# Optimization experiments

Hardware: AMD Instinct MI355X
Metric: run time of the kernel (lower is better)

## Reference

```python
import jax, jax.numpy as jnp
import numpy as np

N = 10000; E = 320000
DIM = 176; ATT = 16; SH_HEADS = 16; TH = 4; NH = SH_HEADS + TH; VD = DIM // SH_HEADS
LMAX = 3; NSPH = (LMAX + 1) ** 2; ZDIM = 16; RDIM = 16
RSTART = 0.8; CUT = 5.0; NLAYERS = 2


def _ln(x):
    mu = jnp.mean(x, axis=-1, keepdims=True)
    dx = x - mu
    var = jnp.mean(dx ** 2, axis=-1, keepdims=True)
    return dx * (1e-6 + var) ** (-0.5)


def _sph(v):
    # real spherical harmonics up to l=3, unnormalized overall scale, [E,16]
    x, y, z = v[..., 0], v[..., 1], v[..., 2]
    s3 = np.float32(np.sqrt(3.0)); s15 = np.float32(np.sqrt(15.0))
    c1 = np.float32(np.sqrt(5.0 / 8.0)); c2 = np.float32(np.sqrt(3.0 / 8.0))
    x2, y2, z2 = x * x, y * y, z * z
    return jnp.stack([
        jnp.ones_like(x),
        x, y, z,
        s3 * x * y, s3 * y * z, 0.5 * (3.0 * z2 - 1.0), s3 * x * z, 0.5 * s3 * (x2 - y2),
        c1 * y * (3.0 * x2 - y2), s15 * x * y * z, c2 * y * (5.0 * z2 - 1.0),
        0.5 * z * (5.0 * z2 - 3.0), c2 * x * (5.0 * z2 - 1.0),
        0.5 * s15 * z * (x2 - y2), c1 * x * (x2 - 3.0 * y2),
    ], axis=-1)


def setup_inputs() -> dict:
    key = jax.random.key(0)
    ks = jax.random.split(key, 32)

    def rn(k, shape):
        fan_in = shape[0] if len(shape) > 1 else shape[0]
        return jax.random.normal(k, shape, dtype=jnp.float32) / np.float32(np.sqrt(shape[0]))

    species = jax.random.randint(ks[0], (N,), 0, 64)
    edge_src = jax.random.randint(ks[1], (E,), 0, N)
    edge_dst = jax.random.randint(ks[2], (E,), 0, N)
    distances = RSTART + (CUT - RSTART) * jax.random.uniform(ks[3], (E,), dtype=jnp.float32)
    raw = jax.random.normal(ks[4], (E, 3), dtype=jnp.float32)
    dirn = raw / jnp.linalg.norm(raw, axis=-1, keepdims=True)
    vec = dirn * distances[:, None]
    switch = 0.5 * (jnp.cos(jnp.pi * distances / CUT) + 1.0)

    inp = {
        'species': species, 'distances': distances, 'switch': switch,
        'edge_src': edge_src, 'edge_dst': edge_dst, 'vec': vec,
        'z_table': jax.random.normal(ks[5], (64, ZDIM), dtype=jnp.float32),
        'w_species': rn(ks[6], (ZDIM, DIM)),
        'pos_w1_0': rn(ks[7], (RDIM, 2 * ATT)), 'pos_b1_0': jnp.zeros((2 * ATT,), jnp.float32),
        'pos_w2_0': rn(ks[8], (2 * ATT, ATT)), 'pos_b2_0': jnp.zeros((ATT,), jnp.float32),
        'wq_0': rn(ks[9], (DIM, NH * ATT)), 'wk_0': rn(ks[10], (DIM, NH * ATT)),
        'wv_0': rn(ks[11], (DIM, SH_HEADS * VD)),
        'upd_w_0': rn(ks[12], (2 * DIM, DIM)), 'upd_b_0': jnp.zeros((DIM,), jnp.float32),
        'pos_w1_1': rn(ks[13], (RDIM + TH * (LMAX + 1), 2 * ATT)), 'pos_b1_1': jnp.zeros((2 * ATT,), jnp.float32),
        'pos_w2_1': rn(ks[14], (2 * ATT, ATT)), 'pos_b2_1': jnp.zeros((ATT,), jnp.float32),
        'wq_1': rn(ks[15], (DIM, NH * ATT)), 'wk_1': rn(ks[16], (DIM, NH * ATT)),
        'wv_1': rn(ks[17], (DIM, SH_HEADS * VD)),
        'upd_w_1': rn(ks[18], (2 * DIM, DIM)), 'upd_b_1': jnp.zeros((DIM,), jnp.float32),
    }
    return inp


def reference(species, distances, switch, edge_src, edge_dst, vec,
              z_table, w_species,
              pos_w1_0, pos_b1_0, pos_w2_0, pos_b2_0, wq_0, wk_0, wv_0, upd_w_0, upd_b_0,
              pos_w1_1, pos_b1_1, pos_w2_1, pos_b2_1, wq_1, wk_1, wv_1, upd_w_1, upd_b_1):
    Nn = species.shape[0]
    Zi = z_table[species]                      # [N, ZDIM] species encoding
    xi = _ln(Zi @ w_species)                   # [N, DIM]

    vhat = vec / distances[:, None]
    Yij = _sph(vhat)                           # [E, NSPH]
    ls = np.repeat(np.arange(LMAX + 1), 2 * np.arange(LMAX + 1) + 1)
    parity = jnp.asarray(((-1.0) ** ls).astype(np.float32))  # [NSPH]

    centers = jnp.linspace(RSTART, CUT, RDIM, dtype=jnp.float32)
    sigma = np.float32((CUT - RSTART) / (RDIM - 1))
    radial = jnp.exp(-(((distances[:, None] - centers) / sigma) ** 2))  # [E, RDIM]

    Vi = jnp.zeros((Nn, TH, NSPH), jnp.float32)
    pos = [(pos_w1_0, pos_b1_0, pos_w2_0, pos_b2_0), (pos_w1_1, pos_b1_1, pos_w2_1, pos_b2_1)]
    att = [(wq_0, wk_0, wv_0, upd_w_0, upd_b_0), (wq_1, wk_1, wv_1, upd_w_1, upd_b_1)]
    inv_sqrt_d = np.float32(1.0 / np.sqrt(ATT))

    for layer in range(NLAYERS):
        pw1, pb1, pw2, pb2 = pos[layer]
        wq, wk, wv, uw, ub = att[layer]
        if layer == 0:
            ur = radial
        else:
            # tensor relative positional features: [E, TH, NSPH]
            xij2 = (Vi[edge_dst] + (parity * Vi)[edge_src]) * Yij[:, None, :]
            us = [xij2[:, :, l * l:(l + 1) * (l + 1)].sum(axis=-1) for l in range(LMAX + 1)]
            ur = jnp.concatenate([radial] + us, axis=-1)
        w = jax.nn.swish(ur @ pw1 + pb1) @ pw2 + pb2     # [E, ATT] positional encoding
        q = (xi @ wq).reshape(Nn, NH, ATT)
        k = (xi @ wk).reshape(Nn, NH, ATT)
        # multiplicative relative positional attention coefficients [E, NH]
        aij = jnp.einsum('ehd,ed->eh', q[edge_dst] * k[edge_src], w) * (switch[:, None] * inv_sqrt_d)
        a_s, a_t = aij[:, :SH_HEADS], aij[:, SH_HEADS:]
        v = (xi @ wv).reshape(Nn, SH_HEADS, VD)
        mi = jax.ops.segment_sum(a_s[:, :, None] * v[edge_src], edge_dst, num_segments=Nn)  # [N,SH,VD]
        Vi = Vi + jax.ops.segment_sum(
            a_t[:, :, None] * (Yij[:, None, :] + parity * Vi[edge_src]), edge_dst, num_segments=Nn)
        ui = jnp.concatenate([xi, mi.reshape(Nn, -1)], axis=-1)
        xi = _ln(xi + ui @ uw + ub)
    return xi
```

## Files before the change

### kernel.cpp

```cpp
#include <hip/hip_runtime.h>
#include <hip/hip_bf16.h>
#include <math.h>

#define N_NODES 10000
#define N_PAD   10048
#define N_EDGES 320000
#define DIM     176
#define ATT     16
#define SH_HEADS 16
#define THH     4
#define NH      20
#define VD      11
#define ZDIM    16
#define RDIM    16
#define QK_W    (NH*ATT)
#define QKV_W   816
#define UI_W    (2*DIM)
#define KQ      192
#define SIGINV  3.5714285714285716f
#define RSTEP   0.28f

typedef unsigned short ushort_t;
typedef __attribute__((ext_vector_type(8))) short bf16x8;
typedef __attribute__((ext_vector_type(4))) float f32x4;


__device__ __forceinline__ ushort_t f2bf(float f) {
    __hip_bfloat16 b = __float2bfloat16(f);
    return *(ushort_t*)&b;
}

__device__ __forceinline__ float bf2f(ushort_t u) {
    return __uint_as_float(((unsigned)u) << 16);
}

__device__ __forceinline__ void sph16(float x, float y, float z, float* Y) {
    const float s3  = 1.7320508075688772f;
    const float s15 = 3.872983346207417f;
    const float c1  = 0.7905694150420949f;
    const float c2  = 0.6123724356957945f;
    float x2 = x*x, y2 = y*y, z2 = z*z;
    Y[0]  = 1.0f;
    Y[1]  = x;
    Y[2]  = y;
    Y[3]  = z;
    Y[4]  = s3 * x * y;
    Y[5]  = s3 * y * z;
    Y[6]  = 0.5f * (3.0f * z2 - 1.0f);
    Y[7]  = s3 * x * z;
    Y[8]  = 0.5f * s3 * (x2 - y2);
    Y[9]  = c1 * y * (3.0f * x2 - y2);
    Y[10] = s15 * x * y * z;
    Y[11] = c2 * y * (5.0f * z2 - 1.0f);
    Y[12] = 0.5f * z * (5.0f * z2 - 3.0f);
    Y[13] = c2 * x * (5.0f * z2 - 1.0f);
    Y[14] = 0.5f * s15 * z * (x2 - y2);
    Y[15] = c1 * x * (x2 - 3.0f * y2);
}

__device__ __forceinline__ void unpack8(const uint4 u, float* f) {
    f[0] = __uint_as_float(u.x << 16);
    f[1] = __uint_as_float(u.x & 0xffff0000u);
    f[2] = __uint_as_float(u.y << 16);
    f[3] = __uint_as_float(u.y & 0xffff0000u);
    f[4] = __uint_as_float(u.z << 16);
    f[5] = __uint_as_float(u.z & 0xffff0000u);
    f[6] = __uint_as_float(u.w << 16);
    f[7] = __uint_as_float(u.w & 0xffff0000u);
}


__global__ __launch_bounds__(256) void k_deg(const int* __restrict__ edst,
        const int* __restrict__ esrc, const float* __restrict__ dist,
        const float* __restrict__ swit, const float* __restrict__ vec,
        int* deg, int* rank, uint4* pk) {
    int e = blockIdx.x * 256 + threadIdx.x;
    if (e >= N_EDGES) return;
    int t_ = edst[e];
    rank[e] = atomicAdd(&deg[t_], 1);
    uint4 a, b;
    a.x = (unsigned)esrc[e];
    a.y = (unsigned)t_;
    a.z = __float_as_uint(dist[e]);
    a.w = __float_as_uint(swit[e]);
    b.x = __float_as_uint(vec[(size_t)e*3 + 0]);
    b.y = __float_as_uint(vec[(size_t)e*3 + 1]);
    b.z = __float_as_uint(vec[(size_t)e*3 + 2]);
    b.w = 0u;
    pk[(size_t)e*2 + 0] = a;
    pk[(size_t)e*2 + 1] = b;
}

__global__ __launch_bounds__(1024) void k_scan1(const int* deg, int* incl, int* bsum) {
    __shared__ int sd[1024];
    int b = blockIdx.x, tid = threadIdx.x;
    int gi = b * 1024 + tid;
    int v = (gi < N_NODES) ? deg[gi] : 0;
    sd[tid] = v;
    __syncthreads();
    for (int s = 1; s < 1024; s <<= 1) {
        int add = (tid >= s) ? sd[tid - s] : 0;
        __syncthreads();
        sd[tid] += add;
        __syncthreads();
    }
    if (gi < N_NODES) incl[gi] = sd[tid];
    if (tid == 1023) bsum[b] = sd[1023];
}

__global__ __launch_bounds__(1024) void k_scan3(const int* deg, const int* incl, const int* bsum,
                                                int* off) {
    __shared__ int bpre_s;
    int b = blockIdx.x, tid = threadIdx.x;
    if (tid == 0) {
        int acc = 0;
        for (int k = 0; k < b; k++) acc += bsum[k];
        bpre_s = acc;
    }
    __syncthreads();
    int gi = b * 1024 + tid;
    if (gi < N_NODES) {
        off[gi + 1] = bpre_s + incl[gi];
    }
    if (gi == 0) off[0] = 0;
}

__global__ __launch_bounds__(256) void k_perm(const int* edst, const int* rank,
                                              const int* off, int* perm) {
    int e = blockIdx.x * 256 + threadIdx.x;
    if (e >= N_EDGES) return;
    perm[off[edst[e]] + rank[e]] = e;
}

__global__ __launch_bounds__(256) void k_build(const int* __restrict__ perm,
        const uint4* __restrict__ pk,
        int* src_c, int* dst_c, float* dist_c, float* sc_c, float* Yf) {
    int p = blockIdx.x * 256 + threadIdx.x;
    if (p >= N_EDGES) return;
    int e  = perm[p];
    uint4 a = pk[(size_t)e*2 + 0];
    uint4 b = pk[(size_t)e*2 + 1];
    int s  = (int)a.x;
    int t_ = (int)a.y;
    float d  = __uint_as_float(a.z);
    float sw = __uint_as_float(a.w);
    float inv = 1.0f / d;
    float vx = __uint_as_float(b.x) * inv;
    float vy = __uint_as_float(b.y) * inv;
    float vz = __uint_as_float(b.z) * inv;
    src_c[p]  = s;
    dst_c[p]  = t_;
    dist_c[p] = d;
    sc_c[p]   = sw * 0.25f;
    float Y[16];
    sph16(vx, vy, vz, Y);
    #pragma unroll
    for (int m = 0; m < 16; m += 4)
        *(float4*)&Yf[(size_t)p * 16 + m] = make_float4(Y[m], Y[m+1], Y[m+2], Y[m+3]);
}


__device__ __forceinline__ void prep_qkv_body(int bid, int tid, const float* wq,
        const float* wk, const float* wv, ushort_t* Wtq) {
    int id = bid * 256 + tid;
    if (id >= 832 * KQ) return;
    int n = id / KQ, k = id - (id / KQ) * KQ;
    float v = 0.0f;
    if (k < DIM && n < QKV_W)
        v = (n < 320) ? wq[k * 320 + n] : (n < 640) ? wk[k * 320 + (n - 320)]
                                                    : wv[k * DIM + (n - 640)];
    Wtq[id] = f2bf(v);
}

__device__ __forceinline__ void prep_upd_body(int bid, int tid, const float* uw, ushort_t* Wtu) {
    int id = bid * 256 + tid;
    if (id >= 192 * UI_W) return;
    int n = id / UI_W, k = id - (id / UI_W) * UI_W;
    float v = (n < DIM) ? uw[k * DIM + n] : 0.0f;
    Wtu[id] = f2bf(v);
}

__device__ __forceinline__ void prep_mlp_body(int bid, int tid, const float* pw1,
        const float* pw2, ushort_t* w1T, ushort_t* w2T, int K1) {
    int id = bid * 256 + tid;
    if (id < 1024) {
        int n = id >> 5, k = id & 31;
        w1T[n * 32 + k] = (k < K1) ? f2bf(pw1[k * 32 + n]) : 0;
    } else if (id < 1536) {
        int id2 = id - 1024;
        int n = id2 >> 5, k = id2 & 31;
        w2T[n * 32 + k] = f2bf(pw2[k * 16 + n]);
    }
}

__global__ __launch_bounds__(256) void k_prep_all(
        const float* wq0, const float* wk0, const float* wv0, ushort_t* Wtq0,
        const float* wq1, const float* wk1, const float* wv1, ushort_t* Wtq1,
        const float* uw0, ushort_t* Wtu0, const float* uw1, ushort_t* Wtu1,
        const float* pw1_0, const float* pw2_0, ushort_t* w1T0, ushort_t* w2T0,
        const float* pw1_1, const float* pw2_1, ushort_t* w1T1, ushort_t* w2T1) {
    int bid = blockIdx.x, tid = threadIdx.x;
    if (bid < 624)        prep_qkv_body(bid,        tid, wq0, wk0, wv0, Wtq0);
    else if (bid < 1248)  prep_qkv_body(bid - 624,  tid, wq1, wk1, wv1, Wtq1);
    else if (bid < 1512)  prep_upd_body(bid - 1248, tid, uw0, Wtu0);
    else if (bid < 1776)  prep_upd_body(bid - 1512, tid, uw1, Wtu1);
    else if (bid < 1782)  prep_mlp_body(bid - 1776, tid, pw1_0, pw2_0, w1T0, w2T0, 16);
    else if (bid < 1788)  prep_mlp_body(bid - 1782, tid, pw1_1, pw2_1, w1T1, w2T1, 32);
}


template<int KCHUNKS>
__global__ __launch_bounds__(256) void k_gemm(const ushort_t* __restrict__ A, int sA,
                                              const ushort_t* __restrict__ Bt, int sB,
                                              float* __restrict__ Cv, int sC, int M, int N) {
    __shared__ ushort_t As[64 * 40];
    __shared__ ushort_t Bs[64 * 40];
    int tid  = threadIdx.x;
    int m0   = blockIdx.y * 64, n0 = blockIdx.x * 64;
    int w    = tid >> 6, lane = tid & 63, quad = lane >> 4, c16 = lane & 15;
    int arow = tid >> 2, aseg = tid & 3;
    f32x4 acc[4] = {};
    for (int kc = 0; kc < KCHUNKS; kc++) {
        int k0 = kc * 32;
        *(uint4*)&As[arow * 40 + aseg * 8] =
            *(const uint4*)&A[(size_t)(m0 + arow) * sA + k0 + aseg * 8];
        *(uint4*)&Bs[arow * 40 + aseg * 8] =
            *(const uint4*)&Bt[(size_t)(n0 + arow) * sB + k0 + aseg * 8];
        __syncthreads();
        bf16x8 a = *(const bf16x8*)&As[(w * 16 + c16) * 40 + quad * 8];
        #pragma unroll
        for (int t = 0; t < 4; t++) {
            bf16x8 b = *(const bf16x8*)&Bs[(t * 16 + c16) * 40 + quad * 8];
            acc[t] = __builtin_amdgcn_mfma_f32_16x16x32_bf16(a, b, acc[t], 0, 0, 0);
        }
        __syncthreads();
    }
    #pragma unroll
    for (int t = 0; t < 4; t++) {
        #pragma unroll
        for (int r = 0; r < 4; r++) {
            int row = m0 + w * 16 + quad * 4 + r;
            int col = n0 + t * 16 + c16;
            if (row < M && col < N)
                Cv[(size_t)row * sC + col] = acc[t][r];
        }
    }
}


__global__ __launch_bounds__(256) void k_gemmq(const ushort_t* __restrict__ A,
                                               const ushort_t* __restrict__ Bt,
                                               ushort_t* __restrict__ qh,
                                               ushort_t* __restrict__ kh,
                                               ushort_t* __restrict__ vh) {
    __shared__ ushort_t As[64 * 200];
    __shared__ ushort_t Bs[64 * 200];
    int tid  = threadIdx.x;
    int m0   = blockIdx.y * 64, n0 = blockIdx.x * 64;
    int w    = tid >> 6, lane = tid & 63, quad = lane >> 4, c16 = lane & 15;
    #pragma unroll
    for (int it = 0; it < 6; it++) {
        int seg = it * 256 + tid;
        int r = seg / 24, cs = seg - (seg / 24) * 24;
        *(uint4*)&As[r * 200 + cs * 8] =
            *(const uint4*)&A[(size_t)(m0 + r) * KQ + cs * 8];
        *(uint4*)&Bs[r * 200 + cs * 8] =
            *(const uint4*)&Bt[(size_t)(n0 + r) * KQ + cs * 8];
    }
    __syncthreads();
    f32x4 acc[4] = {};
    #pragma unroll
    for (int kc = 0; kc < 6; kc++) {
        bf16x8 a = *(const bf16x8*)&As[(w * 16 + c16) * 200 + kc * 32 + quad * 8];
        #pragma unroll
        for (int t = 0; t < 4; t++) {
            bf16x8 b = *(const bf16x8*)&Bs[(t * 16 + c16) * 200 + kc * 32 + quad * 8];
            acc[t] = __builtin_amdgcn_mfma_f32_16x16x32_bf16(a, b, acc[t], 0, 0, 0);
        }
    }
    #pragma unroll
    for (int t = 0; t < 4; t++) {
        #pragma unroll
        for (int r = 0; r < 4; r++) {
            int row = m0 + w * 16 + quad * 4 + r;
            int col = n0 + t * 16 + c16;
            if (row < N_NODES && col < QKV_W) {
                ushort_t bv = f2bf(acc[t][r]);
                if (col < 320)      qh[(size_t)row * QK_W + col] = bv;
                else if (col < 640) kh[(size_t)row * QK_W + (col - 320)] = bv;
                else                vh[(size_t)row * DIM  + (col - 640)] = bv;
            }
        }
    }
}


__global__ __launch_bounds__(256) void k_node_init(const int* species, const float* z_table,
                                                   const float* wsp, float* xi,
                                                   ushort_t* xib, ushort_t* cxm) {
    __shared__ float zs[16 * ZDIM];
    __shared__ float yt[16 * DIM];
    __shared__ float red[256];
    __shared__ float mus[16], rstds[16];
    int base = blockIdx.x * 16;
    int tid  = threadIdx.x;
    { int n = tid >> 4, kk = tid & 15;
      zs[tid] = z_table[species[base + n] * ZDIM + kk]; }
    __syncthreads();
    int c = tid;
    if (c < DIM) {
        float acc[16];
        #pragma unroll
        for (int n = 0; n < 16; n++) acc[n] = 0.0f;
        for (int kk = 0; kk < ZDIM; kk++) {
            float w = wsp[kk * DIM + c];
            #pragma unroll
            for (int n = 0; n < 16; n++) acc[n] += zs[n * ZDIM + kk] * w;
        }
        #pragma unroll
        for (int n = 0; n < 16; n++) yt[n * DIM + c] = acc[n];
    }
    __syncthreads();
    { int n2 = tid >> 4, j = tid & 15;
      float s = 0.0f;
      for (int c2 = j; c2 < DIM; c2 += 16) s += yt[n2 * DIM + c2];
      red[tid] = s; }
    __syncthreads();
    if (tid < 16) { float s = 0; for (int j = 0; j < 16; j++) s += red[tid * 16 + j]; mus[tid] = s / (float)DIM; }
    __syncthreads();
    { int n2 = tid >> 4, j = tid & 15;
      float mu = mus[n2], s = 0.0f;
      for (int c2 = j; c2 < DIM; c2 += 16) { float d = yt[n2 * DIM + c2] - mu; s += d * d; }
      red[tid] = s; }
    __syncthreads();
    if (tid < 16) { float s = 0; for (int j = 0; j < 16; j++) s += red[tid * 16 + j]; rstds[tid] = rsqrtf(s / (float)DIM + 1e-6f); }
    __syncthreads();
    if (c < DIM) {
        #pragma unroll
        for (int n = 0; n < 16; n++) {
            float val = (yt[n * DIM + c] - mus[n]) * rstds[n];
            xi[(size_t)(base + n) * DIM + c] = val;
            ushort_t bv = f2bf(val);
            xib[(size_t)(base + n) * KQ + c]   = bv;
            cxm[(size_t)(base + n) * UI_W + c] = bv;
        }
    } else if (c < KQ) {
        #pragma unroll
        for (int n = 0; n < 16; n++) xib[(size_t)(base + n) * KQ + c] = 0;
    }
}


template<bool L0>
__global__ __launch_bounds__(256) void k_edge(const float* dist_c, const float* sc_c,
        const int* src_c, const int* dst_c, const float* Yf, const ushort_t* Vih,
        const ushort_t* qh, const ushort_t* kh,
        const ushort_t* w1T, const float* pb1, const ushort_t* w2T, const float* pb2,
        ushort_t* aijh) {
    __shared__ ushort_t urS[64 * 40];
    __shared__ ushort_t Ht[4][16 * 40];
    __shared__ float    wdS[64 * 17];
    __shared__ ushort_t aS[NH][64];
    int tid  = threadIdx.x;
    int w    = tid >> 6, lane = tid & 63, quad = lane >> 4, c16 = lane & 15;
    int eb   = blockIdx.x * 64;

    int le = tid >> 2, part = tid & 3;
    int ie = eb + le;
    int sE = src_c[ie], tE = dst_c[ie];

    if (!L0) {
        int e  = tid & 63, tp = tid >> 6;
        int i  = eb + e;
        float d = dist_c[i];
        ushort_t ur4[4];
        #pragma unroll
        for (int r0 = 0; r0 < 4; r0++) {
            int r = tp * 4 + r0;
            float cc = 0.8f + (float)r * RSTEP;
            float uu = (d - cc) * SIGINV;
            ur4[r0] = f2bf(__expf(-uu * uu));
        }
        *(uint2*)&urS[e * 40 + tp * 4] = *(uint2*)ur4;
        float Y[16];
        #pragma unroll
        for (int m = 0; m < 16; m += 4) {
            float4 y = *(const float4*)&Yf[(size_t)i * 16 + m];
            Y[m] = y.x; Y[m+1] = y.y; Y[m+2] = y.z; Y[m+3] = y.w;
        }
        int s = src_c[i], t_ = dst_c[i];
        const uint4* vd4 = (const uint4*)(Vih + (size_t)t_ * 64);
        const uint4* vs4 = (const uint4*)(Vih + (size_t)s  * 64);
        int th = tp;
        float fd[16], fs[16];
        unpack8(vd4[2*th],   fd);     unpack8(vd4[2*th+1], fd+8);
        unpack8(vs4[2*th],   fs);     unpack8(vs4[2*th+1], fs+8);
        float us0 = (fd[0] + fs[0]) * Y[0];
        float us1 = 0.0f, us2 = 0.0f, us3 = 0.0f;
        #pragma unroll
        for (int m = 1; m < 4; m++)  us1 += (fd[m] - fs[m]) * Y[m];
        #pragma unroll
        for (int m = 4; m < 9; m++)  us2 += (fd[m] + fs[m]) * Y[m];
        #pragma unroll
        for (int m = 9; m < 16; m++) us3 += (fd[m] - fs[m]) * Y[m];
        urS[e * 40 + 16 + 0 * 4 + th] = f2bf(us0);
        urS[e * 40 + 16 + 1 * 4 + th] = f2bf(us1);
        urS[e * 40 + 16 + 2 * 4 + th] = f2bf(us2);
        urS[e * 40 + 16 + 3 * 4 + th] = f2bf(us3);
        __syncthreads();
    }

    uint4 kr[10];
    {
        const uint4* kseg = (const uint4*)(kh + (size_t)sE * QK_W) + part * 10;
        #pragma unroll
        for (int j = 0; j < 10; j++) kr[j] = kseg[j];
    }

    {
        int e0 = eb + w * 16;
        bf16x8 a1;
        if (L0) {
            float d = dist_c[e0 + c16];
            #pragma unroll
            for (int j = 0; j < 8; j++) {
                int r = quad * 8 + j;
                float v = 0.0f;
                if (r < 16) { float cc = 0.8f + (float)r * RSTEP; float uu = (d - cc) * SIGINV; v = __expf(-uu * uu); }
                a1[j] = (short)f2bf(v);
            }
        } else {
            a1 = *(const bf16x8*)&urS[(w * 16 + c16) * 40 + quad * 8];
        }
        bf16x8 b0 = *(const bf16x8*)&w1T[c16 * 32 + quad * 8];
        bf16x8 b1 = *(const bf16x8*)&w1T[(16 + c16) * 32 + quad * 8];
        f32x4 acc0 = {}, acc1 = {};
        acc0 = __builtin_amdgcn_mfma_f32_16x16x32_bf16(a1, b0, acc0, 0, 0, 0);
        acc1 = __builtin_amdgcn_mfma_f32_16x16x32_bf16(a1, b1, acc1, 0, 0, 0);
        float bb0 = pb1[c16], bb1 = pb1[c16 + 16];
        #pragma unroll
        for (int r = 0; r < 4; r++) {
            int er = quad * 4 + r;
            float h0 = acc0[r] + bb0; h0 = h0 / (1.0f + __expf(-h0));
            float h1 = acc1[r] + bb1; h1 = h1 / (1.0f + __expf(-h1));
            Ht[w][er * 40 + c16]      = f2bf(h0);
            Ht[w][er * 40 + 16 + c16] = f2bf(h1);
        }
        __syncthreads();
        bf16x8 a2 = *(const bf16x8*)&Ht[w][c16 * 40 + quad * 8];
        bf16x8 b2 = *(const bf16x8*)&w2T[c16 * 32 + quad * 8];
        f32x4 acc2 = {};
        acc2 = __builtin_amdgcn_mfma_f32_16x16x32_bf16(a2, b2, acc2, 0, 0, 0);
        float bb2 = pb2[c16];
        #pragma unroll
        for (int r = 0; r < 4; r++) {
            int er = quad * 4 + r;
            wdS[(w * 16 + er) * 17 + c16] = (acc2[r] + bb2) * sc_c[e0 + er];
        }
    }
    __syncthreads();

    {
        float wd[16];
        #pragma unroll
        for (int p = 0; p < 16; p++) wd[p] = wdS[le * 17 + p];
        const uint4* q4 = (const uint4*)(qh + (size_t)tE * QK_W) + part * 10;
        #pragma unroll
        for (int j = 0; j < 5; j++) {
            int h = part * 5 + j;
            float qa[8], qb[8], ka[8], kb[8];
            unpack8(q4[2*j],   qa); unpack8(q4[2*j+1], qb);
            unpack8(kr[2*j],   ka); unpack8(kr[2*j+1], kb);
            float acc = 0.0f;
            #pragma unroll
            for (int dd = 0; dd < 8; dd++) acc += qa[dd] * ka[dd] * wd[dd];
            #pragma unroll
            for (int dd = 0; dd < 8; dd++) acc += qb[dd] * kb[dd] * wd[8 + dd];
            aS[h][le] = f2bf(acc);
        }
    }
    __syncthreads();
    {
        const uint* aSw = (const uint*)aS;
        for (int idx = tid; idx < NH * 32; idx += 256) {
            int h = idx >> 5, w2 = idx & 31;
            *(uint*)(aijh + (size_t)h * N_EDGES + eb + w2 * 2) = aSw[h * 32 + w2];
        }
    }
}


__device__ __forceinline__ void mi_step(int i, int c0, bool f1, bool f2,
        const int* src_c, const ushort_t* aA, const ushort_t* aB, const ushort_t* vh,
        float& acc0, float& acc1, float& acc2, float& acc3) {
    int s0 = src_c[i];
    uint2 v0 = *(const uint2*)(vh + (size_t)s0 * DIM + c0);
    float a00 = bf2f(aA[i]), a0B = bf2f(aB[i]);
    float g01 = f1 ? a0B : a00, g02 = f2 ? a0B : a00;
    acc0 += a00 * __uint_as_float(v0.x << 16);
    acc1 += g01 * __uint_as_float(v0.x & 0xffff0000u);
    acc2 += g02 * __uint_as_float(v0.y << 16);
    acc3 += a0B * __uint_as_float(v0.y & 0xffff0000u);
}

__device__ __forceinline__ void mi_wave(int n, int lane, const int* off, const int* src_c,
        const ushort_t* aijh, const ushort_t* vh, ushort_t* cxm) {
    if (lane >= 44) return;
    int c0 = lane * 4;
    int hA = c0 / VD;
    int hB = (c0 + 3) / VD;
    bool f1 = ((c0 + 1) / VD) != hA;
    bool f2 = ((c0 + 2) / VD) != hA;
    const ushort_t* aA = aijh + (size_t)hA * N_EDGES;
    const ushort_t* aB = aijh + (size_t)hB * N_EDGES;
    int start = off[n], end = off[n + 1];
    float acc0 = 0, acc1 = 0, acc2 = 0, acc3 = 0;
    int cnt = end - start;
    int i = start;

#define MI_ACC(vv, av, bv) { \
    float aa = bf2f(av), ab = bf2f(bv); \
    float g1 = f1 ? ab : aa, g2 = f2 ? ab : aa; \
    acc0 += aa * __uint_as_float((vv).x << 16); \
    acc1 += g1 * __uint_as_float((vv).x & 0xffff0000u); \
    acc2 += g2 * __uint_as_float((vv).y << 16); \
    acc3 += ab * __uint_as_float((vv).y & 0xffff0000u); }

    if (cnt >= 4) {
        int iend = start + (cnt & ~3);
        int s0 = src_c[i], s1 = src_c[i+1], s2 = src_c[i+2], s3 = src_c[i+3];
        uint2 v0 = *(const uint2*)(vh + (size_t)s0 * DIM + c0);
        uint2 v1 = *(const uint2*)(vh + (size_t)s1 * DIM + c0);
        uint2 v2 = *(const uint2*)(vh + (size_t)s2 * DIM + c0);
        uint2 v3 = *(const uint2*)(vh + (size_t)s3 * DIM + c0);
        ushort_t pA0 = aA[i], pA1 = aA[i+1], pA2 = aA[i+2], pA3 = aA[i+3];
        ushort_t pB0 = aB[i], pB1 = aB[i+1], pB2 = aB[i+2], pB3 = aB[i+3];
        for (i += 4; i + 4 <= iend; i += 4) {
            int t0 = src_c[i], t1 = src_c[i+1], t2 = src_c[i+2], t3 = src_c[i+3];
            uint2 w0 = *(const uint2*)(vh + (size_t)t0 * DIM + c0);
            uint2 w1 = *(const uint2*)(vh + (size_t)t1 * DIM + c0);
            uint2 w2 = *(const uint2*)(vh + (size_t)t2 * DIM + c0);
            uint2 w3 = *(const uint2*)(vh + (size_t)t3 * DIM + c0);
            ushort_t qA0 = aA[i], qA1 = aA[i+1], qA2 = aA[i+2], qA3 = aA[i+3];
            ushort_t qB0 = aB[i], qB1 = aB[i+1], qB2 = aB[i+2], qB3 = aB[i+3];
            MI_ACC(v0, pA0, pB0); MI_ACC(v1, pA1, pB1);
            MI_ACC(v2, pA2, pB2); MI_ACC(v3, pA3, pB3);
            v0 = w0; v1 = w1; v2 = w2; v3 = w3;
            pA0 = qA0; pA1 = qA1; pA2 = qA2; pA3 = qA3;
            pB0 = qB0; pB1 = qB1; pB2 = qB2; pB3 = qB3;
        }
        MI_ACC(v0, pA0, pB0); MI_ACC(v1, pA1, pB1);
        MI_ACC(v2, pA2, pB2); MI_ACC(v3, pA3, pB3);
    }
    for (; i < end; i++)
        mi_step(i, c0, f1, f2, src_c, aA, aB, vh, acc0, acc1, acc2, acc3);
#undef MI_ACC
    ushort_t o[4] = {f2bf(acc0), f2bf(acc1), f2bf(acc2), f2bf(acc3)};
    *(uint2*)(cxm + (size_t)n * UI_W + DIM + c0) = *(uint2*)o;
}

__device__ __forceinline__ void vi_wave(int n, int lane, const int* off,
        const float* Yf, const ushort_t* aijh, ushort_t* Vih) {
    int th = lane >> 4, sm = lane & 15;
    const ushort_t* ah = aijh + (size_t)(SH_HEADS + th) * N_EDGES;
    int start = off[n], end = off[n + 1];
    float acc = 0.0f;
    int cnt = end - start;
    int i = start;
    if (cnt >= 4) {
        int iend = start + (cnt & ~3);
        float a0 = bf2f(ah[i]),   y0 = Yf[(size_t)i * 16 + sm];
        float a1 = bf2f(ah[i+1]), y1 = Yf[(size_t)(i+1) * 16 + sm];
        float a2 = bf2f(ah[i+2]), y2 = Yf[(size_t)(i+2) * 16 + sm];
        float a3 = bf2f(ah[i+3]), y3 = Yf[(size_t)(i+3) * 16 + sm];
        for (i += 4; i + 4 <= iend; i += 4) {
            float b0 = bf2f(ah[i]),   z0 = Yf[(size_t)i * 16 + sm];
            float b1 = bf2f(ah[i+1]), z1 = Yf[(size_t)(i+1) * 16 + sm];
            float b2 = bf2f(ah[i+2]), z2 = Yf[(size_t)(i+2) * 16 + sm];
            float b3 = bf2f(ah[i+3]), z3 = Yf[(size_t)(i+3) * 16 + sm];
            acc += a0 * y0 + a1 * y1 + a2 * y2 + a3 * y3;
            a0 = b0; a1 = b1; a2 = b2; a3 = b3;
            y0 = z0; y1 = z1; y2 = z2; y3 = z3;
        }
        acc += a0 * y0 + a1 * y1 + a2 * y2 + a3 * y3;
    }
    for (; i < end; i++)
        acc += bf2f(ah[i]) * Yf[(size_t)i * 16 + sm];
    Vih[(size_t)n * 64 + lane] = f2bf(acc);
}

__global__ __launch_bounds__(256) void k_agg0(const int* off, const int* src_c,
        const float* Yf, const ushort_t* aijh, const ushort_t* vh,
        ushort_t* cxm, ushort_t* Vih) {
    int wid  = blockIdx.x * 4 + (threadIdx.x >> 6);
    int lane = threadIdx.x & 63;
    if (wid < N_NODES)
        mi_wave(wid, lane, off, src_c, aijh, vh, cxm);
    else
        vi_wave(wid - N_NODES, lane, off, Yf, aijh, Vih);
}

__global__ __launch_bounds__(256) void k_agg1(const int* off, const int* src_c,
        const ushort_t* aijh, const ushort_t* vh, ushort_t* cxm) {
    int wid  = blockIdx.x * 4 + (threadIdx.x >> 6);
    int lane = threadIdx.x & 63;
    mi_wave(wid, lane, off, src_c, aijh, vh, cxm);
}


__global__ __launch_bounds__(256) void k_lnfinal(const float* yg, const float* xi,
        const float* ub, float* xo, ushort_t* xib, ushort_t* cxm) {
    __shared__ float yt[16 * DIM];
    __shared__ float red[256];
    __shared__ float mus[16], rstds[16];
    int base = blockIdx.x * 16;
    int tid  = threadIdx.x;
    for (int idx = tid; idx < 16 * DIM; idx += 256) {
        int n = idx / DIM, c = idx - n * DIM;
        yt[idx] = xi[(size_t)(base + n) * DIM + c]
                + yg[(size_t)(base + n) * DIM + c] + ub[c];
    }
    __syncthreads();
    { int n2 = tid >> 4, j = tid & 15;
      float s = 0.0f;
      for (int c2 = j; c2 < DIM; c2 += 16) s += yt[n2 * DIM + c2];
      red[tid] = s; }
    __syncthreads();
    if (tid < 16) { float s = 0; for (int j = 0; j < 16; j++) s += red[tid * 16 + j]; mus[tid] = s / (float)DIM; }
    __syncthreads();
    { int n2 = tid >> 4, j = tid & 15;
      float mu = mus[n2], s = 0.0f;
      for (int c2 = j; c2 < DIM; c2 += 16) { float d = yt[n2 * DIM + c2] - mu; s += d * d; }
      red[tid] = s; }
    __syncthreads();
    if (tid < 16) { float s = 0; for (int j = 0; j < 16; j++) s += red[tid * 16 + j]; rstds[tid] = rsqrtf(s / (float)DIM + 1e-6f); }
    __syncthreads();
    int c = tid;
    if (c < DIM) {
        #pragma unroll
        for (int n = 0; n < 16; n++) {
            float val = (yt[n * DIM + c] - mus[n]) * rstds[n];
            xo[(size_t)(base + n) * DIM + c] = val;
            ushort_t bv = f2bf(val);
            xib[(size_t)(base + n) * KQ + c]   = bv;
            cxm[(size_t)(base + n) * UI_W + c] = bv;
        }
    } else if (c < KQ) {
        #pragma unroll
        for (int n = 0; n < 16; n++) xib[(size_t)(base + n) * KQ + c] = 0;
    }
}


extern "C" void kernel_launch(void* const* d_in, const int* in_sizes, int n_in,
                              void* d_out, int out_size, void* d_ws, size_t ws_size,
                              hipStream_t stream) {
    const int*   species = (const int*)  d_in[0];
    const float* dist    = (const float*)d_in[1];
    const float* swit    = (const float*)d_in[2];
    const int*   esrc    = (const int*)  d_in[3];
    const int*   edst    = (const int*)  d_in[4];
    const float* vec     = (const float*)d_in[5];
    const float* z_table = (const float*)d_in[6];
    const float* wsp     = (const float*)d_in[7];
    const float* pw1_0 = (const float*)d_in[8],  *pb1_0 = (const float*)d_in[9];
    const float* pw2_0 = (const float*)d_in[10], *pb2_0 = (const float*)d_in[11];
    const float* wq0 = (const float*)d_in[12], *wk0 = (const float*)d_in[13];
    const float* wv0 = (const float*)d_in[14], *uw0 = (const float*)d_in[15];
    const float* ub0 = (const float*)d_in[16];
    const float* pw1_1 = (const float*)d_in[17], *pb1_1 = (const float*)d_in[18];
    const float* pw2_1 = (const float*)d_in[19], *pb2_1 = (const float*)d_in[20];
    const float* wq1 = (const float*)d_in[21], *wk1 = (const float*)d_in[22];
    const float* wv1 = (const float*)d_in[23], *uw1 = (const float*)d_in[24];
    const float* ub1 = (const float*)d_in[25];
    float* out = (float*)d_out;

    char* p = (char*)d_ws;
    auto alloc = [&](size_t bytes) -> char* {
        char* r = p;
        p += (bytes + 255) & ~(size_t)255;
        return r;
    };
    int* deg    = (int*)alloc((size_t)N_NODES * 4);
    int* incl   = (int*)alloc((size_t)N_NODES * 4);
    int* bsum   = (int*)alloc(64);
    int* off    = (int*)alloc((size_t)(N_NODES + 1) * 4);
    int* rank   = (int*)alloc((size_t)N_EDGES * 4);
    int* perm   = (int*)alloc((size_t)N_EDGES * 4);
    uint4* pk   = (uint4*)alloc((size_t)N_EDGES * 32);
    int*   src_c  = (int*)  alloc((size_t)N_EDGES * 4);
    int*   dst_c  = (int*)  alloc((size_t)N_EDGES * 4);
    float* dist_c = (float*)alloc((size_t)N_EDGES * 4);
    float* sc_c   = (float*)alloc((size_t)N_EDGES * 4);
    float* Yf     = (float*)alloc((size_t)N_EDGES * 16 * 4);
    float* xiA  = (float*)alloc((size_t)N_NODES * DIM * 4);
    float* xiB  = (float*)alloc((size_t)N_NODES * DIM * 4);
    ushort_t* xib  = (ushort_t*)alloc((size_t)N_PAD * KQ * 2);
    ushort_t* cxm  = (ushort_t*)alloc((size_t)N_PAD * UI_W * 2);
    ushort_t* qh   = (ushort_t*)alloc((size_t)N_NODES * QK_W * 2);
    ushort_t* kh   = (ushort_t*)alloc((size_t)N_NODES * QK_W * 2);
    ushort_t* vh   = (ushort_t*)alloc((size_t)N_NODES * DIM * 2);
    float* ybuf    = (float*)alloc((size_t)N_NODES * DIM * 4);
    ushort_t* Wtq0 = (ushort_t*)alloc((size_t)832 * KQ * 2);
    ushort_t* Wtq1 = (ushort_t*)alloc((size_t)832 * KQ * 2);
    ushort_t* Wtu0 = (ushort_t*)alloc((size_t)192 * UI_W * 2);
    ushort_t* Wtu1 = (ushort_t*)alloc((size_t)192 * UI_W * 2);
    ushort_t* w1T0 = (ushort_t*)alloc((size_t)32 * 32 * 2);
    ushort_t* w2T0 = (ushort_t*)alloc((size_t)16 * 32 * 2);
    ushort_t* w1T1 = (ushort_t*)alloc((size_t)32 * 32 * 2);
    ushort_t* w2T1 = (ushort_t*)alloc((size_t)16 * 32 * 2);
    ushort_t* Vih  = (ushort_t*)alloc((size_t)N_NODES * 64 * 2);
    ushort_t* aijh = (ushort_t*)alloc((size_t)N_EDGES * NH * 2);

    const int NB_E  = (N_EDGES + 255) / 256;
    const int NB_F  = N_EDGES / 64;
    const int NB_T  = N_NODES / 16;
    const dim3 GRID_QKV(13, 157);
    const dim3 GRID_UPD(3, 157);

    hipMemsetAsync(deg, 0, (size_t)N_NODES * 4, stream);
    k_deg<<<NB_E, 256, 0, stream>>>(edst, esrc, dist, swit, vec, deg, rank, pk);
    k_scan1<<<10, 1024, 0, stream>>>(deg, incl, bsum);
    k_scan3<<<10, 1024, 0, stream>>>(deg, incl, bsum, off);
    k_perm<<<NB_E, 256, 0, stream>>>(edst, rank, off, perm);
    k_build<<<NB_E, 256, 0, stream>>>(perm, pk, src_c, dst_c, dist_c, sc_c, Yf);

    k_prep_all<<<1788, 256, 0, stream>>>(wq0, wk0, wv0, Wtq0, wq1, wk1, wv1, Wtq1,
                                         uw0, Wtu0, uw1, Wtu1,
                                         pw1_0, pw2_0, w1T0, w2T0,
                                         pw1_1, pw2_1, w1T1, w2T1);

    k_node_init<<<NB_T, 256, 0, stream>>>(species, z_table, wsp, xiA, xib, cxm);

    k_gemmq<<<GRID_QKV, 256, 0, stream>>>(xib, Wtq0, qh, kh, vh);
    k_edge<true><<<NB_F, 256, 0, stream>>>(dist_c, sc_c, src_c, dst_c, Yf, Vih,
                                           qh, kh, w1T0, pb1_0, w2T0, pb2_0, aijh);
    k_agg0<<<5000, 256, 0, stream>>>(off, src_c, Yf, aijh, vh, cxm, Vih);
    k_gemm<11><<<GRID_UPD, 256, 0, stream>>>(cxm, UI_W, Wtu0, UI_W, ybuf, DIM,
                                             N_NODES, DIM);
    k_lnfinal<<<NB_T, 256, 0, stream>>>(ybuf, xiA, ub0, xiB, xib, cxm);

    k_gemmq<<<GRID_QKV, 256, 0, stream>>>(xib, Wtq1, qh, kh, vh);
    k_edge<false><<<NB_F, 256, 0, stream>>>(dist_c, sc_c, src_c, dst_c, Yf, Vih,
                                            qh, kh, w1T1, pb1_1, w2T1, pb2_1, aijh);
    k_agg1<<<2500, 256, 0, stream>>>(off, src_c, aijh, vh, cxm);
    k_gemm<11><<<GRID_UPD, 256, 0, stream>>>(cxm, UI_W, Wtu1, UI_W, ybuf, DIM,
                                             N_NODES, DIM);
    k_lnfinal<<<NB_T, 256, 0, stream>>>(ybuf, xiB, ub1, out, xib, cxm);
}
```

Before: 373.1 us.

## Fuse update GEMM with layernorm, merge preprocessing launches, single-block scan

The node-update GEMM and the residual layernorm become one kernel, k_updln. Each 64-row block stages its A rows in LDS, runs MFMA over all 176 output columns, and does the mean and variance reduction with lane shuffles. This removes the fp32 ybuf round trip and one launch per layer. Degree counting, weight prep and node init are merged into one multi-role kernel, and the two-kernel scan becomes a single 1024-thread block. The trade-offs: k_updln launches only 157 blocks and reads B straight from global memory, and every block of the merged pre-kernel reserves the init LDS.

```diff
diff --git a/kernel.cpp b/kernel.cpp
--- a/kernel.cpp
+++ b/kernel.cpp
@@ -70,11 +70,11 @@
 }
 
 
-__global__ __launch_bounds__(256) void k_deg(const int* __restrict__ edst,
-        const int* __restrict__ esrc, const float* __restrict__ dist,
-        const float* __restrict__ swit, const float* __restrict__ vec,
-        int* deg, int* rank, uint4* pk) {
-    int e = blockIdx.x * 256 + threadIdx.x;
+__device__ __forceinline__ void deg_body(int bid, int tid,
+        const int* __restrict__ edst, const int* __restrict__ esrc,
+        const float* __restrict__ dist, const float* __restrict__ swit,
+        const float* __restrict__ vec, int* deg, int* rank, uint4* pk) {
+    int e = bid * 256 + tid;
     if (e >= N_EDGES) return;
     int t_ = edst[e];
     rank[e] = atomicAdd(&deg[t_], 1);
@@ -91,38 +91,147 @@
     pk[(size_t)e*2 + 1] = b;
 }
 
-__global__ __launch_bounds__(1024) void k_scan1(const int* deg, int* incl, int* bsum) {
+__device__ __forceinline__ void prep_qkv_body(int bid, int tid, const float* wq,
+        const float* wk, const float* wv, ushort_t* Wtq) {
+    int id = bid * 256 + tid;
+    if (id >= 832 * KQ) return;
+    int n = id / KQ, k = id - (id / KQ) * KQ;
+    float v = 0.0f;
+    if (k < DIM && n < QKV_W)
+        v = (n < 320) ? wq[k * 320 + n] : (n < 640) ? wk[k * 320 + (n - 320)]
+                                                    : wv[k * DIM + (n - 640)];
+    Wtq[id] = f2bf(v);
+}
+
+__device__ __forceinline__ void prep_upd_body(int bid, int tid, const float* uw, ushort_t* Wtu) {
+    int id = bid * 256 + tid;
+    if (id >= 192 * UI_W) return;
+    int n = id / UI_W, k = id - (id / UI_W) * UI_W;
+    float v = (n < DIM) ? uw[k * DIM + n] : 0.0f;
+    Wtu[id] = f2bf(v);
+}
+
+__device__ __forceinline__ void prep_mlp_body(int bid, int tid, const float* pw1,
+        const float* pw2, ushort_t* w1T, ushort_t* w2T, int K1) {
+    int id = bid * 256 + tid;
+    if (id < 1024) {
+        int n = id >> 5, k = id & 31;
+        w1T[n * 32 + k] = (k < K1) ? f2bf(pw1[k * 32 + n]) : 0;
+    } else if (id < 1536) {
+        int id2 = id - 1024;
+        int n = id2 >> 5, k = id2 & 31;
+        w2T[n * 32 + k] = f2bf(pw2[k * 16 + n]);
+    }
+}
+
+struct InitSmem {
+    float zs[16 * ZDIM];
+    float yt[16 * DIM];
+    float red[256];
+    float mus[16], rstds[16];
+};
+
+__device__ void init_body(int bid, int tid, InitSmem& sm,
+        const int* species, const float* z_table, const float* wsp,
+        float* xi, ushort_t* xib, ushort_t* cxm) {
+    int base = bid * 16;
+    { int n = tid >> 4, kk = tid & 15;
+      sm.zs[tid] = z_table[species[base + n] * ZDIM + kk]; }
+    __syncthreads();
+    int c = tid;
+    if (c < DIM) {
+        float acc[16];
+        #pragma unroll
+        for (int n = 0; n < 16; n++) acc[n] = 0.0f;
+        for (int kk = 0; kk < ZDIM; kk++) {
+            float w = wsp[kk * DIM + c];
+            #pragma unroll
+            for (int n = 0; n < 16; n++) acc[n] += sm.zs[n * ZDIM + kk] * w;
+        }
+        #pragma unroll
+        for (int n = 0; n < 16; n++) sm.yt[n * DIM + c] = acc[n];
+    }
+    __syncthreads();
+    { int n2 = tid >> 4, j = tid & 15;
+      float s = 0.0f;
+      for (int c2 = j; c2 < DIM; c2 += 16) s += sm.yt[n2 * DIM + c2];
+      sm.red[tid] = s; }
+    __syncthreads();
+    if (tid < 16) { float s = 0; for (int j = 0; j < 16; j++) s += sm.red[tid * 16 + j]; sm.mus[tid] = s / (float)DIM; }
+    __syncthreads();
+    { int n2 = tid >> 4, j = tid & 15;
+      float mu = sm.mus[n2], s = 0.0f;
+      for (int c2 = j; c2 < DIM; c2 += 16) { float d = sm.yt[n2 * DIM + c2] - mu; s += d * d; }
+      sm.red[tid] = s; }
+    __syncthreads();
+    if (tid < 16) { float s = 0; for (int j = 0; j < 16; j++) s += sm.red[tid * 16 + j]; sm.rstds[tid] = rsqrtf(s / (float)DIM + 1e-6f); }
+    __syncthreads();
+    if (c < DIM) {
+        #pragma unroll
+        for (int n = 0; n < 16; n++) {
+            float val = (sm.yt[n * DIM + c] - sm.mus[n]) * sm.rstds[n];
+            xi[(size_t)(base + n) * DIM + c] = val;
+            ushort_t bv = f2bf(val);
+            xib[(size_t)(base + n) * KQ + c]   = bv;
+            cxm[(size_t)(base + n) * UI_W + c] = bv;
+        }
+    } else if (c < KQ) {
+        #pragma unroll
+        for (int n = 0; n < 16; n++) xib[(size_t)(base + n) * KQ + c] = 0;
+    }
+}
+
+__global__ __launch_bounds__(256) void k_pre(
+        const int* edst, const int* esrc, const float* dist, const float* swit,
+        const float* vec, int* deg, int* rank, uint4* pk,
+        const float* wq0, const float* wk0, const float* wv0, ushort_t* Wtq0,
+        const float* wq1, const float* wk1, const float* wv1, ushort_t* Wtq1,
+        const float* uw0, ushort_t* Wtu0, const float* uw1, ushort_t* Wtu1,
+        const float* pw1_0, const float* pw2_0, ushort_t* w1T0, ushort_t* w2T0,
+        const float* pw1_1, const float* pw2_1, ushort_t* w1T1, ushort_t* w2T1,
+        const int* species, const float* z_table, const float* wsp,
+        float* xi, ushort_t* xib, ushort_t* cxm) {
+    __shared__ InitSmem sm;
+    int bid = blockIdx.x, tid = threadIdx.x;
+    if (bid < 1250)       deg_body(bid, tid, edst, esrc, dist, swit, vec, deg, rank, pk);
+    else if (bid < 1874)  prep_qkv_body(bid - 1250, tid, wq0, wk0, wv0, Wtq0);
+    else if (bid < 2498)  prep_qkv_body(bid - 1874, tid, wq1, wk1, wv1, Wtq1);
+    else if (bid < 2762)  prep_upd_body(bid - 2498, tid, uw0, Wtu0);
+    else if (bid < 3026)  prep_upd_body(bid - 2762, tid, uw1, Wtu1);
+    else if (bid < 3032)  prep_mlp_body(bid - 3026, tid, pw1_0, pw2_0, w1T0, w2T0, 16);
+    else if (bid < 3038)  prep_mlp_body(bid - 3032, tid, pw1_1, pw2_1, w1T1, w2T1, 32);
+    else                  init_body(bid - 3038, tid, sm, species, z_table, wsp, xi, xib, cxm);
+}
+
+
+__global__ __launch_bounds__(1024) void k_scan(const int* __restrict__ deg, int* off) {
     __shared__ int sd[1024];
-    int b = blockIdx.x, tid = threadIdx.x;
-    int gi = b * 1024 + tid;
-    int v = (gi < N_NODES) ? deg[gi] : 0;
-    sd[tid] = v;
-    __syncthreads();
-    for (int s = 1; s < 1024; s <<= 1) {
-        int add = (tid >= s) ? sd[tid - s] : 0;
+    int tid = threadIdx.x;
+    int base = tid * 10;
+    int v[10];
+    int s = 0;
+    #pragma unroll
+    for (int j = 0; j < 10; j++) {
+        int gi = base + j;
+        v[j] = (gi < N_NODES) ? deg[gi] : 0;
+        s += v[j];
+    }
+    sd[tid] = s;
+    __syncthreads();
+    for (int st = 1; st < 1024; st <<= 1) {
+        int add = (tid >= st) ? sd[tid - st] : 0;
         __syncthreads();
         sd[tid] += add;
         __syncthreads();
     }
-    if (gi < N_NODES) incl[gi] = sd[tid];
-    if (tid == 1023) bsum[b] = sd[1023];
-}
-
-__global__ __launch_bounds__(1024) void k_scan3(const int* deg, const int* incl, const int* bsum,
-                                                int* off) {
-    __shared__ int bpre_s;
-    int b = blockIdx.x, tid = threadIdx.x;
-    if (tid == 0) {
-        int acc = 0;
-        for (int k = 0; k < b; k++) acc += bsum[k];
-        bpre_s = acc;
-    }
-    __syncthreads();
-    int gi = b * 1024 + tid;
-    if (gi < N_NODES) {
-        off[gi + 1] = bpre_s + incl[gi];
-    }
-    if (gi == 0) off[0] = 0;
+    int run = (tid > 0) ? sd[tid - 1] : 0;
+    #pragma unroll
+    for (int j = 0; j < 10; j++) {
+        run += v[j];
+        int gi = base + j;
+        if (gi < N_NODES) off[gi + 1] = run;
+    }
+    if (tid == 0) off[0] = 0;
 }
 
 __global__ __launch_bounds__(256) void k_perm(const int* edst, const int* rank,
@@ -160,94 +269,6 @@
 }
 
 
-__device__ __forceinline__ void prep_qkv_body(int bid, int tid, const float* wq,
-        const float* wk, const float* wv, ushort_t* Wtq) {
-    int id = bid * 256 + tid;
-    if (id >= 832 * KQ) return;
-    int n = id / KQ, k = id - (id / KQ) * KQ;
-    float v = 0.0f;
-    if (k < DIM && n < QKV_W)
-        v = (n < 320) ? wq[k * 320 + n] : (n < 640) ? wk[k * 320 + (n - 320)]
-                                                    : wv[k * DIM + (n - 640)];
-    Wtq[id] = f2bf(v);
-}
-
-__device__ __forceinline__ void prep_upd_body(int bid, int tid, const float* uw, ushort_t* Wtu) {
-    int id = bid * 256 + tid;
-    if (id >= 192 * UI_W) return;
-    int n = id / UI_W, k = id - (id / UI_W) * UI_W;
-    float v = (n < DIM) ? uw[k * DIM + n] : 0.0f;
-    Wtu[id] = f2bf(v);
-}
-
-__device__ __forceinline__ void prep_mlp_body(int bid, int tid, const float* pw1,
-        const float* pw2, ushort_t* w1T, ushort_t* w2T, int K1) {
-    int id = bid * 256 + tid;
-    if (id < 1024) {
-        int n = id >> 5, k = id & 31;
-        w1T[n * 32 + k] = (k < K1) ? f2bf(pw1[k * 32 + n]) : 0;
-    } else if (id < 1536) {
-        int id2 = id - 1024;
-        int n = id2 >> 5, k = id2 & 31;
-        w2T[n * 32 + k] = f2bf(pw2[k * 16 + n]);
-    }
-}
-
-__global__ __launch_bounds__(256) void k_prep_all(
-        const float* wq0, const float* wk0, const float* wv0, ushort_t* Wtq0,
-        const float* wq1, const float* wk1, const float* wv1, ushort_t* Wtq1,
-        const float* uw0, ushort_t* Wtu0, const float* uw1, ushort_t* Wtu1,
-        const float* pw1_0, const float* pw2_0, ushort_t* w1T0, ushort_t* w2T0,
-        const float* pw1_1, const float* pw2_1, ushort_t* w1T1, ushort_t* w2T1) {
-    int bid = blockIdx.x, tid = threadIdx.x;
-    if (bid < 624)        prep_qkv_body(bid,        tid, wq0, wk0, wv0, Wtq0);
-    else if (bid < 1248)  prep_qkv_body(bid - 624,  tid, wq1, wk1, wv1, Wtq1);
-    else if (bid < 1512)  prep_upd_body(bid - 1248, tid, uw0, Wtu0);
-    else if (bid < 1776)  prep_upd_body(bid - 1512, tid, uw1, Wtu1);
-    else if (bid < 1782)  prep_mlp_body(bid - 1776, tid, pw1_0, pw2_0, w1T0, w2T0, 16);
-    else if (bid < 1788)  prep_mlp_body(bid - 1782, tid, pw1_1, pw2_1, w1T1, w2T1, 32);
-}
-
-
-template<int KCHUNKS>
-__global__ __launch_bounds__(256) void k_gemm(const ushort_t* __restrict__ A, int sA,
-                                              const ushort_t* __restrict__ Bt, int sB,
-                                              float* __restrict__ Cv, int sC, int M, int N) {
-    __shared__ ushort_t As[64 * 40];
-    __shared__ ushort_t Bs[64 * 40];
-    int tid  = threadIdx.x;
-    int m0   = blockIdx.y * 64, n0 = blockIdx.x * 64;
-    int w    = tid >> 6, lane = tid & 63, quad = lane >> 4, c16 = lane & 15;
-    int arow = tid >> 2, aseg = tid & 3;
-    f32x4 acc[4] = {};
-    for (int kc = 0; kc < KCHUNKS; kc++) {
-        int k0 = kc * 32;
-        *(uint4*)&As[arow * 40 + aseg * 8] =
-            *(const uint4*)&A[(size_t)(m0 + arow) * sA + k0 + aseg * 8];
-        *(uint4*)&Bs[arow * 40 + aseg * 8] =
-            *(const uint4*)&Bt[(size_t)(n0 + arow) * sB + k0 + aseg * 8];
-        __syncthreads();
-        bf16x8 a = *(const bf16x8*)&As[(w * 16 + c16) * 40 + quad * 8];
-        #pragma unroll
-        for (int t = 0; t < 4; t++) {
-            bf16x8 b = *(const bf16x8*)&Bs[(t * 16 + c16) * 40 + quad * 8];
-            acc[t] = __builtin_amdgcn_mfma_f32_16x16x32_bf16(a, b, acc[t], 0, 0, 0);
-        }
-        __syncthreads();
-    }
-    #pragma unroll
-    for (int t = 0; t < 4; t++) {
-        #pragma unroll
-        for (int r = 0; r < 4; r++) {
-            int row = m0 + w * 16 + quad * 4 + r;
-            int col = n0 + t * 16 + c16;
-            if (row < M && col < N)
-                Cv[(size_t)row * sC + col] = acc[t][r];
-        }
-    }
-}
-
-
 __global__ __launch_bounds__(256) void k_gemmq(const ushort_t* __restrict__ A,
                                                const ushort_t* __restrict__ Bt,
                                                ushort_t* __restrict__ qh,
@@ -295,58 +316,68 @@
 }
 
 
-__global__ __launch_bounds__(256) void k_node_init(const int* species, const float* z_table,
-                                                   const float* wsp, float* xi,
-                                                   ushort_t* xib, ushort_t* cxm) {
-    __shared__ float zs[16 * ZDIM];
-    __shared__ float yt[16 * DIM];
-    __shared__ float red[256];
-    __shared__ float mus[16], rstds[16];
-    int base = blockIdx.x * 16;
+__global__ __launch_bounds__(256) void k_updln(const ushort_t* __restrict__ A,
+        const ushort_t* __restrict__ Bt, const float* __restrict__ xi,
+        const float* __restrict__ ub,
+        float* xo, ushort_t* xib, ushort_t* cxm) {
+    __shared__ ushort_t As[64 * 360];
     int tid  = threadIdx.x;
-    { int n = tid >> 4, kk = tid & 15;
-      zs[tid] = z_table[species[base + n] * ZDIM + kk]; }
-    __syncthreads();
-    int c = tid;
-    if (c < DIM) {
-        float acc[16];
-        #pragma unroll
-        for (int n = 0; n < 16; n++) acc[n] = 0.0f;
-        for (int kk = 0; kk < ZDIM; kk++) {
-            float w = wsp[kk * DIM + c];
-            #pragma unroll
-            for (int n = 0; n < 16; n++) acc[n] += zs[n * ZDIM + kk] * w;
-        }
-        #pragma unroll
-        for (int n = 0; n < 16; n++) yt[n * DIM + c] = acc[n];
-    }
-    __syncthreads();
-    { int n2 = tid >> 4, j = tid & 15;
-      float s = 0.0f;
-      for (int c2 = j; c2 < DIM; c2 += 16) s += yt[n2 * DIM + c2];
-      red[tid] = s; }
-    __syncthreads();
-    if (tid < 16) { float s = 0; for (int j = 0; j < 16; j++) s += red[tid * 16 + j]; mus[tid] = s / (float)DIM; }
-    __syncthreads();
-    { int n2 = tid >> 4, j = tid & 15;
-      float mu = mus[n2], s = 0.0f;
-      for (int c2 = j; c2 < DIM; c2 += 16) { float d = yt[n2 * DIM + c2] - mu; s += d * d; }
-      red[tid] = s; }
-    __syncthreads();
-    if (tid < 16) { float s = 0; for (int j = 0; j < 16; j++) s += red[tid * 16 + j]; rstds[tid] = rsqrtf(s / (float)DIM + 1e-6f); }
-    __syncthreads();
-    if (c < DIM) {
-        #pragma unroll
-        for (int n = 0; n < 16; n++) {
-            float val = (yt[n * DIM + c] - mus[n]) * rstds[n];
-            xi[(size_t)(base + n) * DIM + c] = val;
-            ushort_t bv = f2bf(val);
-            xib[(size_t)(base + n) * KQ + c]   = bv;
-            cxm[(size_t)(base + n) * UI_W + c] = bv;
-        }
-    } else if (c < KQ) {
-        #pragma unroll
-        for (int n = 0; n < 16; n++) xib[(size_t)(base + n) * KQ + c] = 0;
+    int m0   = blockIdx.x * 64;
+    int w    = tid >> 6, lane = tid & 63, quad = lane >> 4, c16 = lane & 15;
+    #pragma unroll
+    for (int it = 0; it < 11; it++) {
+        int seg = it * 256 + tid;
+        int r = seg / 44, cs = seg - (seg / 44) * 44;
+        *(uint4*)&As[r * 360 + cs * 8] =
+            *(const uint4*)&A[(size_t)(m0 + r) * UI_W + cs * 8];
+    }
+    __syncthreads();
+    f32x4 acc[11] = {};
+    for (int kc = 0; kc < 11; kc++) {
+        bf16x8 a = *(const bf16x8*)&As[(w * 16 + c16) * 360 + kc * 32 + quad * 8];
+        #pragma unroll
+        for (int t = 0; t < 11; t++) {
+            bf16x8 b = *(const bf16x8*)&Bt[(size_t)(t * 16 + c16) * UI_W + kc * 32 + quad * 8];
+            acc[t] = __builtin_amdgcn_mfma_f32_16x16x32_bf16(a, b, acc[t], 0, 0, 0);
+        }
+    }
+    float ubv[11];
+    #pragma unroll
+    for (int t = 0; t < 11; t++) ubv[t] = ub[t * 16 + c16];
+    int rowb = m0 + w * 16 + quad * 4;
+    #pragma unroll
+    for (int r = 0; r < 4; r++) {
+        int row = rowb + r;
+        if (row >= N_NODES) continue;
+        float srow = 0.0f;
+        #pragma unroll
+        for (int t = 0; t < 11; t++) {
+            float val = acc[t][r] + xi[(size_t)row * DIM + t * 16 + c16] + ubv[t];
+            acc[t][r] = val;
+            srow += val;
+        }
+        srow += __shfl_xor(srow, 1);
+        srow += __shfl_xor(srow, 2);
+        srow += __shfl_xor(srow, 4);
+        srow += __shfl_xor(srow, 8);
+        float mu = srow / (float)DIM;
+        float sv = 0.0f;
+        #pragma unroll
+        for (int t = 0; t < 11; t++) { float d = acc[t][r] - mu; sv += d * d; }
+        sv += __shfl_xor(sv, 1);
+        sv += __shfl_xor(sv, 2);
+        sv += __shfl_xor(sv, 4);
+        sv += __shfl_xor(sv, 8);
+        float rstd = rsqrtf(sv / (float)DIM + 1e-6f);
+        #pragma unroll
+        for (int t = 0; t < 11; t++) {
+            int col = t * 16 + c16;
+            float nv = (acc[t][r] - mu) * rstd;
+            xo[(size_t)row * DIM + col] = nv;
+            ushort_t bv = f2bf(nv);
+            xib[(size_t)row * KQ + col]   = bv;
+            cxm[(size_t)row * UI_W + col] = bv;
+        }
     }
 }
 
@@ -608,50 +639,6 @@
 }
 
 
-__global__ __launch_bounds__(256) void k_lnfinal(const float* yg, const float* xi,
-        const float* ub, float* xo, ushort_t* xib, ushort_t* cxm) {
-    __shared__ float yt[16 * DIM];
-    __shared__ float red[256];
-    __shared__ float mus[16], rstds[16];
-    int base = blockIdx.x * 16;
-    int tid  = threadIdx.x;
-    for (int idx = tid; idx < 16 * DIM; idx += 256) {
-        int n = idx / DIM, c = idx - n * DIM;
-        yt[idx] = xi[(size_t)(base + n) * DIM + c]
-                + yg[(size_t)(base + n) * DIM + c] + ub[c];
-    }
-    __syncthreads();
-    { int n2 = tid >> 4, j = tid & 15;
-      float s = 0.0f;
-      for (int c2 = j; c2 < DIM; c2 += 16) s += yt[n2 * DIM + c2];
-      red[tid] = s; }
-    __syncthreads();
-    if (tid < 16) { float s = 0; for (int j = 0; j < 16; j++) s += red[tid * 16 + j]; mus[tid] = s / (float)DIM; }
-    __syncthreads();
-    { int n2 = tid >> 4, j = tid & 15;
-      float mu = mus[n2], s = 0.0f;
-      for (int c2 = j; c2 < DIM; c2 += 16) { float d = yt[n2 * DIM + c2] - mu; s += d * d; }
-      red[tid] = s; }
-    __syncthreads();
-    if (tid < 16) { float s = 0; for (int j = 0; j < 16; j++) s += red[tid * 16 + j]; rstds[tid] = rsqrtf(s / (float)DIM + 1e-6f); }
-    __syncthreads();
-    int c = tid;
-    if (c < DIM) {
-        #pragma unroll
-        for (int n = 0; n < 16; n++) {
-            float val = (yt[n * DIM + c] - mus[n]) * rstds[n];
-            xo[(size_t)(base + n) * DIM + c] = val;
-            ushort_t bv = f2bf(val);
-            xib[(size_t)(base + n) * KQ + c]   = bv;
-            cxm[(size_t)(base + n) * UI_W + c] = bv;
-        }
-    } else if (c < KQ) {
-        #pragma unroll
-        for (int n = 0; n < 16; n++) xib[(size_t)(base + n) * KQ + c] = 0;
-    }
-}
-
-
 extern "C" void kernel_launch(void* const* d_in, const int* in_sizes, int n_in,
                               void* d_out, int out_size, void* d_ws, size_t ws_size,
                               hipStream_t stream) {
@@ -682,8 +669,6 @@
         return r;
     };
     int* deg    = (int*)alloc((size_t)N_NODES * 4);
-    int* incl   = (int*)alloc((size_t)N_NODES * 4);
-    int* bsum   = (int*)alloc(64);
     int* off    = (int*)alloc((size_t)(N_NODES + 1) * 4);
     int* rank   = (int*)alloc((size_t)N_EDGES * 4);
     int* perm   = (int*)alloc((size_t)N_EDGES * 4);
@@ -700,7 +685,6 @@
     ushort_t* qh   = (ushort_t*)alloc((size_t)N_NODES * QK_W * 2);
     ushort_t* kh   = (ushort_t*)alloc((size_t)N_NODES * QK_W * 2);
     ushort_t* vh   = (ushort_t*)alloc((size_t)N_NODES * DIM * 2);
-    float* ybuf    = (float*)alloc((size_t)N_NODES * DIM * 4);
     ushort_t* Wtq0 = (ushort_t*)alloc((size_t)832 * KQ * 2);
     ushort_t* Wtq1 = (ushort_t*)alloc((size_t)832 * KQ * 2);
     ushort_t* Wtu0 = (ushort_t*)alloc((size_t)192 * UI_W * 2);
@@ -714,37 +698,28 @@
 
     const int NB_E  = (N_EDGES + 255) / 256;
     const int NB_F  = N_EDGES / 64;
-    const int NB_T  = N_NODES / 16;
     const dim3 GRID_QKV(13, 157);
-    const dim3 GRID_UPD(3, 157);
 
     hipMemsetAsync(deg, 0, (size_t)N_NODES * 4, stream);
-    k_deg<<<NB_E, 256, 0, stream>>>(edst, esrc, dist, swit, vec, deg, rank, pk);
-    k_scan1<<<10, 1024, 0, stream>>>(deg, incl, bsum);
-    k_scan3<<<10, 1024, 0, stream>>>(deg, incl, bsum, off);
+    k_pre<<<3663, 256, 0, stream>>>(edst, esrc, dist, swit, vec, deg, rank, pk,
+                                    wq0, wk0, wv0, Wtq0, wq1, wk1, wv1, Wtq1,
+                                    uw0, Wtu0, uw1, Wtu1,
+                                    pw1_0, pw2_0, w1T0, w2T0,
+                                    pw1_1, pw2_1, w1T1, w2T1,
+                                    species, z_table, wsp, xiA, xib, cxm);
+    k_scan<<<1, 1024, 0, stream>>>(deg, off);
     k_perm<<<NB_E, 256, 0, stream>>>(edst, rank, off, perm);
     k_build<<<NB_E, 256, 0, stream>>>(perm, pk, src_c, dst_c, dist_c, sc_c, Yf);
-
-    k_prep_all<<<1788, 256, 0, stream>>>(wq0, wk0, wv0, Wtq0, wq1, wk1, wv1, Wtq1,
-                                         uw0, Wtu0, uw1, Wtu1,
-                                         pw1_0, pw2_0, w1T0, w2T0,
-                                         pw1_1, pw2_1, w1T1, w2T1);
-
-    k_node_init<<<NB_T, 256, 0, stream>>>(species, z_table, wsp, xiA, xib, cxm);
 
     k_gemmq<<<GRID_QKV, 256, 0, stream>>>(xib, Wtq0, qh, kh, vh);
     k_edge<true><<<NB_F, 256, 0, stream>>>(dist_c, sc_c, src_c, dst_c, Yf, Vih,
                                            qh, kh, w1T0, pb1_0, w2T0, pb2_0, aijh);
     k_agg0<<<5000, 256, 0, stream>>>(off, src_c, Yf, aijh, vh, cxm, Vih);
-    k_gemm<11><<<GRID_UPD, 256, 0, stream>>>(cxm, UI_W, Wtu0, UI_W, ybuf, DIM,
-                                             N_NODES, DIM);
-    k_lnfinal<<<NB_T, 256, 0, stream>>>(ybuf, xiA, ub0, xiB, xib, cxm);
+    k_updln<<<157, 256, 0, stream>>>(cxm, Wtu0, xiA, ub0, xiB, xib, cxm);
 
     k_gemmq<<<GRID_QKV, 256, 0, stream>>>(xib, Wtq1, qh, kh, vh);
     k_edge<false><<<NB_F, 256, 0, stream>>>(dist_c, sc_c, src_c, dst_c, Yf, Vih,
                                             qh, kh, w1T1, pb1_1, w2T1, pb2_1, aijh);
     k_agg1<<<2500, 256, 0, stream>>>(off, src_c, aijh, vh, cxm);
-    k_gemm<11><<<GRID_UPD, 256, 0, stream>>>(cxm, UI_W, Wtu1, UI_W, ybuf, DIM,
-                                             N_NODES, DIM);
-    k_lnfinal<<<NB_T, 256, 0, stream>>>(ybuf, xiB, ub1, out, xib, cxm);
-}
+    k_updln<<<157, 256, 0, stream>>>(cxm, Wtu1, xiB, ub1, out, xib, cxm);
+}
```

Result: slower. 388.4 us (+4.1%).
